# Kernel tuning notes

Measured on AMD Instinct MI355X. Metric: run time of the kernel, lower is better.

The kernel has to match this reference:

```python
import math
import jax, jax.numpy as jnp
import numpy as np

EMBED_DIM = 128
NUM_HEADS = 2
B, N = 4096, 32  # batch of fully-connected ally graphs, N allies each (self-edges included)


def sparsemax(z, axis):
    """Sparsemax (Martins & Astudillo 2016) along `axis`."""
    K = z.shape[axis]
    z_sorted = -jnp.sort(-z, axis=axis)  # descending
    z_cumsum = jnp.cumsum(z_sorted, axis=axis)
    shape = [1] * z.ndim
    shape[axis] = K
    k = jnp.arange(1, K + 1, dtype=z.dtype).reshape(shape)
    support = (1.0 + k * z_sorted) > z_cumsum
    k_sup = jnp.sum(support.astype(z.dtype), axis=axis, keepdims=True)
    tau = (jnp.sum(jnp.where(support, z_sorted, 0.0), axis=axis, keepdims=True) - 1.0) / k_sup
    return jnp.maximum(z - tau, 0.0)


def setup_inputs() -> dict:
    key = jax.random.key(0)
    k1, k2, k3, k4 = jax.random.split(key, 4)
    D, H = EMBED_DIM, NUM_HEADS
    node_feature = jax.random.normal(k1, (B, N, D), dtype=jnp.float32)
    scale = 1.0 / math.sqrt(D)
    WK = jax.random.normal(k2, (D, H * D), dtype=jnp.float32) * scale
    WV = jax.random.normal(k3, (D, H * D), dtype=jnp.float32) * scale
    WQ = jax.random.normal(k4, (D, H * D), dtype=jnp.float32) * scale
    return {"node_feature": node_feature, "WK": WK, "WV": WV, "WQ": WQ}


def reference(node_feature, WK, WV, WQ):
    D, H = EMBED_DIM, NUM_HEADS
    x = node_feature  # [B, N, D]
    # per-node projections; Linear(D, H*D) reshaped to (H, D) as in torch .view
    k = (x @ WK).reshape(B, N, H, D)
    v = (x @ WV).reshape(B, N, H, D)
    q = (x @ WQ).reshape(B, N, H, D)
    # fully connected graph: node i attends over mailbox of all nodes j in same graph
    score = jnp.einsum("bihd,bjhd->bijh", q, k) / math.sqrt(D * H)  # [B, N(i), N(j), H]
    w = sparsemax(score, axis=2)  # sparsemax over neighbor (mailbox) dim
    out = jnp.einsum("bijh,bjhd->bihd", w, v)  # weighted reduction
    out = out.mean(axis=2)  # mean over heads -> [B, N, D]
    output = out.reshape(B * N, D)
    # weight padded to max_num_allies (= N here, so no extra padding needed)
    weight = w.reshape(B * N, N, H)
    return output, weight
```

## Files before the change

kernel.cpp:

```cpp
#include <hip/hip_runtime.h>
#include <hip/hip_bf16.h>


#define NG 4096

typedef short bf16x8 __attribute__((ext_vector_type(8)));
typedef float f32x4 __attribute__((ext_vector_type(4)));

__device__ inline short f2bf(float f) {
    __hip_bfloat16 h = __float2bfloat16(f);
    return __builtin_bit_cast(short, h);
}
__device__ inline unsigned pack2(float a, float b) {
    return (unsigned)(unsigned short)f2bf(a) | ((unsigned)(unsigned short)f2bf(b) << 16);
}

__global__ void pack_mv_kernel(const float* __restrict__ WQ, const float* __restrict__ WK,
                               const float* __restrict__ WV,
                               short* __restrict__ pm, short* __restrict__ pv) {
    int gidx = blockIdx.x * 256 + threadIdx.x;
    if (gidx < 32768) {
        int idx  = gidx;
        int jj   = idx & 7;
        int lane = (idx >> 3) & 63;
        int s    = (idx >> 9) & 3;
        int mt   = (idx >> 11) & 15;
        int h    = mt >> 3;
        int a    = s * 32 + (lane >> 4) * 8 + jj;
        int bl   = (mt & 7) * 16 + (lane & 15);
        const float4* qa = (const float4*)(WQ + a * 256 + h * 128);
        const float4* kb = (const float4*)(WK + bl * 256 + h * 128);
        float acc = 0.f;
        #pragma unroll 8
        for (int c = 0; c < 32; ++c) {
            float4 q4 = qa[c], k4 = kb[c];
            acc += q4.x * k4.x + q4.y * k4.y + q4.z * k4.z + q4.w * k4.w;
        }
        pm[idx] = f2bf(acc * 0.0625f);
    } else {
        int idx  = gidx - 32768;
        int jj   = idx & 7;
        int lane = (idx >> 3) & 63;
        int s    = (idx >> 9) & 3;
        int t    = (idx >> 11) & 15;
        int krow = s * 32 + (lane >> 4) * 8 + jj;
        int col  = t * 16 + (lane & 15);
        pv[idx] = f2bf(WV[krow * 256 + col]);
    }
}

__global__ __launch_bounds__(256, 4)
void fused_attn_kernel(const float* __restrict__ x, const short* __restrict__ pm,
                       const short* __restrict__ pv, float* __restrict__ out,
                       float* __restrict__ wgt) {
    __shared__ char __align__(16) smem[37376];
    short* t_s  = (short*)smem;
    float* s_s  = (float*)smem;
    short* vT_s = (short*)(smem + 16896);

    int b    = blockIdx.x;
    int tid  = threadIdx.x;
    int lane = tid & 63;
    int wave = tid >> 6;
    int lrow = lane & 15;
    int quad = lane >> 4;

    bf16x8 xf[2][4];
    const float* xg = x + (size_t)b * 4096;
    #pragma unroll
    for (int nt = 0; nt < 2; ++nt)
        #pragma unroll
        for (int s = 0; s < 4; ++s) {
            const float* p0 = &xg[(nt * 16 + lrow) * 128 + s * 32 + quad * 8];
            float4 f0 = *(const float4*)p0;
            float4 f1 = *(const float4*)(p0 + 4);
            bf16x8 v;
            v[0]=f2bf(f0.x); v[1]=f2bf(f0.y); v[2]=f2bf(f0.z); v[3]=f2bf(f0.w);
            v[4]=f2bf(f1.x); v[5]=f2bf(f1.y); v[6]=f2bf(f1.z); v[7]=f2bf(f1.w);
            xf[nt][s] = v;
        }

    #pragma unroll
    for (int t = 0; t < 4; ++t) {
        int mt = wave * 4 + t;
        const short* pb = pm + (mt * 4) * 512 + lane * 8;
        bf16x8 wf[4];
        #pragma unroll
        for (int s = 0; s < 4; ++s) wf[s] = *(const bf16x8*)&pb[s * 512];
        f32x4 acc[2] = {{0.f,0.f,0.f,0.f},{0.f,0.f,0.f,0.f}};
        #pragma unroll
        for (int nt = 0; nt < 2; ++nt)
            #pragma unroll
            for (int s = 0; s < 4; ++s)
                acc[nt] = __builtin_amdgcn_mfma_f32_16x16x32_bf16(wf[s], xf[nt][s], acc[nt], 0, 0, 0);
        #pragma unroll
        for (int nt = 0; nt < 2; ++nt) {
            int addr = (nt * 16 + lrow) * 264 + mt * 16 + quad * 4;
            uint2 pk; pk.x = pack2(acc[nt][0], acc[nt][1]); pk.y = pack2(acc[nt][2], acc[nt][3]);
            *(uint2*)&t_s[addr] = pk;
        }
    }
    #pragma unroll
    for (int t = 0; t < 4; ++t) {
        int ntv = wave * 4 + t;
        const short* pb = pv + (ntv * 4) * 512 + lane * 8;
        bf16x8 wf[4];
        #pragma unroll
        for (int s = 0; s < 4; ++s) wf[s] = *(const bf16x8*)&pb[s * 512];
        f32x4 acc[2] = {{0.f,0.f,0.f,0.f},{0.f,0.f,0.f,0.f}};
        #pragma unroll
        for (int mt = 0; mt < 2; ++mt)
            #pragma unroll
            for (int s = 0; s < 4; ++s)
                acc[mt] = __builtin_amdgcn_mfma_f32_16x16x32_bf16(xf[mt][s], wf[s], acc[mt], 0, 0, 0);
        #pragma unroll
        for (int mt = 0; mt < 2; ++mt) {
            int addr = (ntv * 16 + lrow) * 40 + mt * 16 + quad * 4;
            uint2 pk; pk.x = pack2(acc[mt][0], acc[mt][1]); pk.y = pack2(acc[mt][2], acc[mt][3]);
            *(uint2*)&vT_s[addr] = pk;
        }
    }
    __syncthreads();

    f32x4 sacc[2];
    #pragma unroll
    for (int tt = 0; tt < 2; ++tt) {
        int ti = wave * 2 + tt;
        int h = ti >> 2, it = (ti >> 1) & 1, jt = ti & 1;
        f32x4 acc = {0.f, 0.f, 0.f, 0.f};
        #pragma unroll
        for (int s = 0; s < 4; ++s) {
            bf16x8 at = *(const bf16x8*)&t_s[(it * 16 + lrow) * 264 + h * 128 + s * 32 + quad * 8];
            acc = __builtin_amdgcn_mfma_f32_16x16x32_bf16(at, xf[jt][s], acc, 0, 0, 0);
        }
        sacc[tt] = acc;
    }
    __syncthreads();

    #pragma unroll
    for (int tt = 0; tt < 2; ++tt) {
        int ti = wave * 2 + tt;
        int h = ti >> 2, it = (ti >> 1) & 1, jt = ti & 1;
        #pragma unroll
        for (int r = 0; r < 4; ++r)
            s_s[(h * 32 + it * 16 + quad * 4 + r) * 36 + jt * 16 + lrow] = sacc[tt][r];
    }
    __syncthreads();

    {
        int j  = lane & 31;
        int hh = lane >> 5;
        #pragma unroll
        for (int ii = 0; ii < 8; ++ii) {
            int i   = wave * 8 + ii;
            int row = hh * 32 + i;
            const float* zr = &s_s[row * 36];
            float z[32];
            #pragma unroll
            for (int c = 0; c < 8; ++c) {
                float4 f = *(const float4*)&zr[c * 4];
                z[c*4] = f.x; z[c*4+1] = f.y; z[c*4+2] = f.z; z[c*4+3] = f.w;
            }
            float zj = zr[j];
            float c0 = 0.f, c1 = 0.f, s0 = 0.f, s1 = 0.f;
            #pragma unroll
            for (int l = 0; l < 32; l += 2) {
                float m0 = (z[l]     > zj) ? 1.f : 0.f;
                float m1 = (z[l + 1] > zj) ? 1.f : 0.f;
                c0 += m0;  s0 = __builtin_fmaf(m0, z[l],     s0);
                c1 += m1;  s1 = __builtin_fmaf(m1, z[l + 1], s1);
            }
            float rk  = c0 + c1 + 1.f;
            float cum = s0 + s1 + zj;
            float tc  = (cum - 1.f) / rk;
            #pragma unroll
            for (int m = 1; m <= 16; m <<= 1) tc = fmaxf(tc, __shfl_xor(tc, m, 32));
            float w = fmaxf(zj - tc, 0.f);
            ((short*)zr)[j] = f2bf(w);
            float wo = __shfl_xor(w, 32);
            if (lane < 32) {
                float2 v; v.x = w; v.y = wo;
                *(float2*)&wgt[((size_t)b * 32 + i) * 64 + j * 2] = v;
            }
        }
    }
    __syncthreads();

    #pragma unroll
    for (int tt = 0; tt < 4; ++tt) {
        int ti = wave * 4 + tt;
        int it = ti >> 3, dt = ti & 7;
        f32x4 acc = {0.f, 0.f, 0.f, 0.f};
        #pragma unroll
        for (int h = 0; h < 2; ++h) {
            bf16x8 aw = *(const bf16x8*)((short*)&s_s[(h * 32 + it * 16 + lrow) * 36] + quad * 8);
            bf16x8 bv = *(const bf16x8*)&vT_s[(h * 128 + dt * 16 + lrow) * 40 + quad * 8];
            acc = __builtin_amdgcn_mfma_f32_16x16x32_bf16(aw, bv, acc, 0, 0, 0);
        }
        #pragma unroll
        for (int r = 0; r < 4; ++r)
            out[((size_t)b * 32 + it * 16 + quad * 4 + r) * 128 + dt * 16 + lrow] = acc[r] * 0.5f;
    }
}

extern "C" void kernel_launch(void* const* d_in, const int* in_sizes, int n_in,
                              void* d_out, int out_size, void* d_ws, size_t ws_size,
                              hipStream_t stream) {
    const float* x  = (const float*)d_in[0];
    const float* WK = (const float*)d_in[1];
    const float* WV = (const float*)d_in[2];
    const float* WQ = (const float*)d_in[3];
    float* out = (float*)d_out;
    float* wgt = out + (size_t)NG * 32 * 128;
    short* pm = (short*)d_ws;
    short* pv = pm + 32768;

    hipLaunchKernelGGL(pack_mv_kernel, dim3(256), dim3(256), 0, stream, WQ, WK, WV, pm, pv);
    hipLaunchKernelGGL(fused_attn_kernel, dim3(NG), dim3(256), 0, stream, x, pm, pv, out, wgt);
}
```

Before: 201.8 us.

## Give each wave a private head/row-tile to drop block barriers and swizzle LDS

Each wave now computes the Q·M projection only for its own head and node-tile, keeps it in a wave-private LDS region, and immediately computes its score tile and sparsemax without block-wide barriers. Three of the four __syncthreads are removed, LDS footprint shrinks (allowing more resident blocks), and V^T and T buffers use XOR swizzles in place of padding to avoid bank conflicts. The weight output is now written with scalar stores per head instead of paired float2 stores, which may reduce store coalescing.

```diff
diff --git a/kernel.cpp b/kernel.cpp
--- a/kernel.cpp
+++ b/kernel.cpp
@@ -14,6 +14,9 @@
 __device__ inline unsigned pack2(float a, float b) {
     return (unsigned)(unsigned short)f2bf(a) | ((unsigned)(unsigned short)f2bf(b) << 16);
 }
+
+#define VSWZ(row, col) ((((row) << 5) + (col)) ^ (((row) & 3) << 3))
+#define TSWZ(lrow, col) (((lrow) << 7) + (((col) ^ (((lrow) & 7) << 3))))
 
 __global__ void pack_mv_kernel(const float* __restrict__ WQ, const float* __restrict__ WK,
                                const float* __restrict__ WV,
@@ -53,10 +56,9 @@
 void fused_attn_kernel(const float* __restrict__ x, const short* __restrict__ pm,
                        const short* __restrict__ pv, float* __restrict__ out,
                        float* __restrict__ wgt) {
-    __shared__ char __align__(16) smem[37376];
-    short* t_s  = (short*)smem;
-    float* s_s  = (float*)smem;
-    short* vT_s = (short*)(smem + 16896);
+    __shared__ char __align__(16) smem[30720];
+    short* vT_s = (short*)smem;
+    short* w_s = (short*)(smem + 25600);
 
     int b    = blockIdx.x;
     int tid  = threadIdx.x;
@@ -64,42 +66,69 @@
     int wave = tid >> 6;
     int lrow = lane & 15;
     int quad = lane >> 4;
+    int h    = wave >> 1;
+    int nt   = wave & 1;
+
+    short* t_l = (short*)(smem + wave * 4096);
+    float* s_l = (float*)(smem + 16384 + wave * 2304);
 
     bf16x8 xf[2][4];
     const float* xg = x + (size_t)b * 4096;
     #pragma unroll
-    for (int nt = 0; nt < 2; ++nt)
+    for (int ntl = 0; ntl < 2; ++ntl)
         #pragma unroll
         for (int s = 0; s < 4; ++s) {
-            const float* p0 = &xg[(nt * 16 + lrow) * 128 + s * 32 + quad * 8];
+            const float* p0 = &xg[(ntl * 16 + lrow) * 128 + s * 32 + quad * 8];
             float4 f0 = *(const float4*)p0;
             float4 f1 = *(const float4*)(p0 + 4);
             bf16x8 v;
             v[0]=f2bf(f0.x); v[1]=f2bf(f0.y); v[2]=f2bf(f0.z); v[3]=f2bf(f0.w);
             v[4]=f2bf(f1.x); v[5]=f2bf(f1.y); v[6]=f2bf(f1.z); v[7]=f2bf(f1.w);
-            xf[nt][s] = v;
-        }
-
-    #pragma unroll
-    for (int t = 0; t < 4; ++t) {
-        int mt = wave * 4 + t;
-        const short* pb = pm + (mt * 4) * 512 + lane * 8;
-        bf16x8 wf[4];
-        #pragma unroll
-        for (int s = 0; s < 4; ++s) wf[s] = *(const bf16x8*)&pb[s * 512];
-        f32x4 acc[2] = {{0.f,0.f,0.f,0.f},{0.f,0.f,0.f,0.f}};
-        #pragma unroll
-        for (int nt = 0; nt < 2; ++nt)
+            xf[ntl][s] = v;
+        }
+
+    bf16x8 af[4];
+    #pragma unroll
+    for (int half = 0; half < 2; ++half) {
+        f32x4 tacc[4];
+        #pragma unroll
+        for (int t = 0; t < 4; ++t) {
+            int dt = half * 4 + t;
+            int mt = h * 8 + dt;
+            const short* pb = pm + (mt * 4) * 512 + lane * 8;
+            bf16x8 wf[4];
+            #pragma unroll
+            for (int s = 0; s < 4; ++s) wf[s] = *(const bf16x8*)&pb[s * 512];
+            f32x4 acc = {0.f, 0.f, 0.f, 0.f};
             #pragma unroll
             for (int s = 0; s < 4; ++s)
-                acc[nt] = __builtin_amdgcn_mfma_f32_16x16x32_bf16(wf[s], xf[nt][s], acc[nt], 0, 0, 0);
-        #pragma unroll
-        for (int nt = 0; nt < 2; ++nt) {
-            int addr = (nt * 16 + lrow) * 264 + mt * 16 + quad * 4;
-            uint2 pk; pk.x = pack2(acc[nt][0], acc[nt][1]); pk.y = pack2(acc[nt][2], acc[nt][3]);
-            *(uint2*)&t_s[addr] = pk;
-        }
-    }
+                acc = __builtin_amdgcn_mfma_f32_16x16x32_bf16(wf[s], xf[nt][s], acc, 0, 0, 0);
+            tacc[t] = acc;
+        }
+        #pragma unroll
+        for (int t = 0; t < 4; ++t) {
+            int dt = half * 4 + t;
+            uint2 pk; pk.x = pack2(tacc[t][0], tacc[t][1]); pk.y = pack2(tacc[t][2], tacc[t][3]);
+            *(uint2*)&t_l[TSWZ(lrow, dt * 16 + quad * 4)] = pk;
+        }
+        #pragma unroll
+        for (int sc = 0; sc < 2; ++sc) {
+            int s = half * 2 + sc;
+            af[s] = *(const bf16x8*)&t_l[TSWZ(lrow, s * 32 + quad * 8)];
+        }
+    }
+
+    #pragma unroll
+    for (int jt = 0; jt < 2; ++jt) {
+        f32x4 acc = {0.f, 0.f, 0.f, 0.f};
+        #pragma unroll
+        for (int s = 0; s < 4; ++s)
+            acc = __builtin_amdgcn_mfma_f32_16x16x32_bf16(af[s], xf[jt][s], acc, 0, 0, 0);
+        #pragma unroll
+        for (int r = 0; r < 4; ++r)
+            s_l[(quad * 4 + r) * 36 + jt * 16 + lrow] = acc[r];
+    }
+
     #pragma unroll
     for (int t = 0; t < 4; ++t) {
         int ntv = wave * 4 + t;
@@ -109,52 +138,25 @@
         for (int s = 0; s < 4; ++s) wf[s] = *(const bf16x8*)&pb[s * 512];
         f32x4 acc[2] = {{0.f,0.f,0.f,0.f},{0.f,0.f,0.f,0.f}};
         #pragma unroll
-        for (int mt = 0; mt < 2; ++mt)
+        for (int mt2 = 0; mt2 < 2; ++mt2)
             #pragma unroll
             for (int s = 0; s < 4; ++s)
-                acc[mt] = __builtin_amdgcn_mfma_f32_16x16x32_bf16(xf[mt][s], wf[s], acc[mt], 0, 0, 0);
-        #pragma unroll
-        for (int mt = 0; mt < 2; ++mt) {
-            int addr = (ntv * 16 + lrow) * 40 + mt * 16 + quad * 4;
-            uint2 pk; pk.x = pack2(acc[mt][0], acc[mt][1]); pk.y = pack2(acc[mt][2], acc[mt][3]);
-            *(uint2*)&vT_s[addr] = pk;
-        }
-    }
-    __syncthreads();
-
-    f32x4 sacc[2];
-    #pragma unroll
-    for (int tt = 0; tt < 2; ++tt) {
-        int ti = wave * 2 + tt;
-        int h = ti >> 2, it = (ti >> 1) & 1, jt = ti & 1;
-        f32x4 acc = {0.f, 0.f, 0.f, 0.f};
-        #pragma unroll
-        for (int s = 0; s < 4; ++s) {
-            bf16x8 at = *(const bf16x8*)&t_s[(it * 16 + lrow) * 264 + h * 128 + s * 32 + quad * 8];
-            acc = __builtin_amdgcn_mfma_f32_16x16x32_bf16(at, xf[jt][s], acc, 0, 0, 0);
-        }
-        sacc[tt] = acc;
-    }
-    __syncthreads();
-
-    #pragma unroll
-    for (int tt = 0; tt < 2; ++tt) {
-        int ti = wave * 2 + tt;
-        int h = ti >> 2, it = (ti >> 1) & 1, jt = ti & 1;
-        #pragma unroll
-        for (int r = 0; r < 4; ++r)
-            s_s[(h * 32 + it * 16 + quad * 4 + r) * 36 + jt * 16 + lrow] = sacc[tt][r];
-    }
-    __syncthreads();
+                acc[mt2] = __builtin_amdgcn_mfma_f32_16x16x32_bf16(xf[mt2][s], wf[s], acc[mt2], 0, 0, 0);
+        #pragma unroll
+        for (int mt2 = 0; mt2 < 2; ++mt2) {
+            int row = ntv * 16 + lrow;
+            uint2 pk; pk.x = pack2(acc[mt2][0], acc[mt2][1]); pk.y = pack2(acc[mt2][2], acc[mt2][3]);
+            *(uint2*)&vT_s[VSWZ(row, mt2 * 16 + quad * 4)] = pk;
+        }
+    }
 
     {
         int j  = lane & 31;
         int hh = lane >> 5;
         #pragma unroll
         for (int ii = 0; ii < 8; ++ii) {
-            int i   = wave * 8 + ii;
-            int row = hh * 32 + i;
-            const float* zr = &s_s[row * 36];
+            int lr = hh * 8 + ii;
+            const float* zr = &s_l[lr * 36];
             float z[32];
             #pragma unroll
             for (int c = 0; c < 8; ++c) {
@@ -176,12 +178,9 @@
             #pragma unroll
             for (int m = 1; m <= 16; m <<= 1) tc = fmaxf(tc, __shfl_xor(tc, m, 32));
             float w = fmaxf(zj - tc, 0.f);
-            ((short*)zr)[j] = f2bf(w);
-            float wo = __shfl_xor(w, 32);
-            if (lane < 32) {
-                float2 v; v.x = w; v.y = wo;
-                *(float2*)&wgt[((size_t)b * 32 + i) * 64 + j * 2] = v;
-            }
+            w_s[(wave * 16 + lr) * 40 + j] = f2bf(w);
+            int node = nt * 16 + lr;
+            wgt[((size_t)b * 32 + node) * 64 + j * 2 + h] = w;
         }
     }
     __syncthreads();
@@ -192,9 +191,9 @@
         int it = ti >> 3, dt = ti & 7;
         f32x4 acc = {0.f, 0.f, 0.f, 0.f};
         #pragma unroll
-        for (int h = 0; h < 2; ++h) {
-            bf16x8 aw = *(const bf16x8*)((short*)&s_s[(h * 32 + it * 16 + lrow) * 36] + quad * 8);
-            bf16x8 bv = *(const bf16x8*)&vT_s[(h * 128 + dt * 16 + lrow) * 40 + quad * 8];
+        for (int h2 = 0; h2 < 2; ++h2) {
+            bf16x8 aw = *(const bf16x8*)&w_s[(h2 * 32 + it * 16 + lrow) * 40 + quad * 8];
+            bf16x8 bv = *(const bf16x8*)&vT_s[VSWZ(h2 * 128 + dt * 16 + lrow, quad * 8)];
             acc = __builtin_amdgcn_mfma_f32_16x16x32_bf16(aw, bv, acc, 0, 0, 0);
         }
         #pragma unroll
```

New measurement: 267.1 us. 32.4% more time.
